# Performance work log

Measured on AMD Instinct MI355X. Metric: run time of the kernel, lower is better.

## Reference

```python
import jax, jax.numpy as jnp
import numpy as np

S, B, I, H, O = 1024, 64, 512, 2048, 512


def setup_inputs() -> dict:
    key = jax.random.key(0)
    k1, k2, k3, k4, k5 = jax.random.split(key, 5)
    X = jax.random.normal(k1, (S, B, I), dtype=jnp.float32)
    W_ih = jax.random.normal(k2, (H, I), dtype=jnp.float32) * (1.0 / np.sqrt(I))
    hh = jax.random.uniform(k3, (H,), dtype=jnp.float32)  # clamped-to-[-1,1] diagonal recurrence
    W_ho = jax.random.normal(k4, (O, H), dtype=jnp.float32) * (1.0 / np.sqrt(H))
    b_ho = jax.random.normal(k5, (O,), dtype=jnp.float32) * 0.01
    return {"X": X, "W_ih": W_ih, "hh": hh, "W_ho": W_ho, "b_ho": b_ho}


def reference(X, W_ih, hh, W_ho, b_ho):
    # Batch the input->hidden projection over the whole sequence in one GEMM:
    # u[s,b,h] = X[s,b,i] @ W_ih[h,i]^T
    u = jnp.einsum('sbi,hi->sbh', X, W_ih)
    h0 = jnp.zeros((X.shape[1], W_ih.shape[0]), dtype=X.dtype)

    def step(h, u_t):
        h_new = jnp.abs(u_t + hh * h)
        return h_new, None

    h_final, _ = jax.lax.scan(step, h0, u)
    Y = h_final @ W_ho.T + b_ho  # [B, O]
    return Y
```

## Files before the change

### kernel.cpp

```cpp
#include <hip/hip_runtime.h>
#include <hip/hip_bf16.h>
#include <stdint.h>

#define S_LEN 1024
#define B_SZ  64
#define I_SZ  512
#define H_SZ  2048
#define O_SZ  512
#define BH    (B_SZ * H_SZ)

typedef __bf16  bf16x8 __attribute__((ext_vector_type(8)));
typedef float   f32x4  __attribute__((ext_vector_type(4)));

static __device__ __forceinline__ ushort f2bf(float f) {
  union { float f; unsigned u; } v; v.f = f;
  unsigned r = v.u + 0x7FFFu + ((v.u >> 16) & 1u);
  return (ushort)(r >> 16);
}
static __device__ __forceinline__ float bf2f(ushort u) {
  return __builtin_bit_cast(float, (unsigned)u << 16);
}

#define GLOAD_LDS16(gp, lp) \
  __builtin_amdgcn_global_load_lds( \
      (__attribute__((address_space(1))) void*)(gp), \
      (__attribute__((address_space(3))) void*)(lp), 16, 0, 0)

__global__ __launch_bounds__(256) void convert_f32_bf16_kernel(
    const float4* __restrict__ in, ushort4* __restrict__ out, int n4) {
  int i = blockIdx.x * 256 + threadIdx.x;
  if (i >= n4) return;
  float4 v = in[i];
  ushort4 o; o.x = f2bf(v.x); o.y = f2bf(v.y); o.z = f2bf(v.z); o.w = f2bf(v.w);
  out[i] = o;
}

__global__ __launch_bounds__(256, 4) void fused_gemm_scan_kernel(
    const ushort* __restrict__ Xbf,
    const ushort* __restrict__ Wbf,
    const float* __restrict__ hh,
    float* __restrict__ hstate) {
  __shared__ __align__(16) ushort smem[16896];
  ushort* As = smem;
  ushort* Bs = smem + 8192;
  ushort* Cs = smem;

  const int tid  = threadIdx.x;
  const int wave = tid >> 6;
  const int lane = tid & 63;

  const int bid = blockIdx.x;
  const int x = bid & 7;
  const int g = bid >> 3;
  const int b  = (x << 3) | (g & 7);
  const int ht = g >> 3;

  const int wm = (wave >> 1) * 64;
  const int wn = (wave & 1) * 64;
  const int ml = lane & 15;
  const int q  = lane >> 4;

  const int r0     = wave * 32;
  const int srow   = lane >> 3;
  const int schunk = ((lane & 7) - srow) & 7;
  const ushort* gA0 = Xbf + ((size_t)(r0 + srow) * B_SZ + b) * I_SZ + schunk * 8;
  const ushort* gB  = Wbf + (size_t)(ht * 128 + r0 + srow) * I_SZ + schunk * 8;
  ushort* lA = As + r0 * 64;
  ushort* lB = Bs + r0 * 64;

  int swz[2];
  swz[0] = ((q + ml) & 7) * 8;
  swz[1] = ((4 + q + ml) & 7) * 8;
  int arow[4], brow[4];
  #pragma unroll
  for (int i = 0; i < 4; ++i) {
    arow[i] = (wm + i * 16 + ml) * 64;
    brow[i] = (wn + i * 16 + ml) * 64;
  }

  float c = 0.0f, hst = 0.0f;
  if (tid < 128) c = hh[ht * 128 + tid];

  for (int st = 0; st < 8; ++st) {
    f32x4 acc[4][4] = {};
    const ushort* gA = gA0 + (size_t)st * 128 * B_SZ * I_SZ;

    for (int kt = 0; kt < I_SZ / 64; ++kt) {
      __syncthreads();
      #pragma unroll
      for (int jj = 0; jj < 4; ++jj) {
        GLOAD_LDS16(gA + (size_t)(jj * 8) * B_SZ * I_SZ + kt * 64, lA + jj * 512);
        GLOAD_LDS16(gB + (size_t)(jj * 8) * I_SZ + kt * 64, lB + jj * 512);
      }
      __syncthreads();
      #pragma unroll
      for (int ks = 0; ks < 2; ++ks) {
        bf16x8 af[4], bfr[4];
        #pragma unroll
        for (int i = 0; i < 4; ++i) {
          af[i]  = *(const bf16x8*)&As[arow[i] + swz[ks]];
          bfr[i] = *(const bf16x8*)&Bs[brow[i] + swz[ks]];
        }
        #pragma unroll
        for (int mi = 0; mi < 4; ++mi)
          #pragma unroll
          for (int ni = 0; ni < 4; ++ni)
            acc[mi][ni] = __builtin_amdgcn_mfma_f32_16x16x32_bf16(
                af[mi], bfr[ni], acc[mi][ni], 0, 0, 0);
      }
    }

    __syncthreads();
    const int rl0 = wm + q * 4;
    #pragma unroll
    for (int mi = 0; mi < 4; ++mi)
      #pragma unroll
      for (int ni = 0; ni < 4; ++ni)
        #pragma unroll
        for (int r = 0; r < 4; ++r)
          Cs[(rl0 + mi * 16 + r) * 132 + wn + ni * 16 + ml] = f2bf(acc[mi][ni][r]);
    __syncthreads();

    if (tid < 128) {
      #pragma unroll
      for (int s8 = 0; s8 < 128; s8 += 8) {
        float uv[8];
        #pragma unroll
        for (int t = 0; t < 8; ++t) uv[t] = bf2f(Cs[(s8 + t) * 132 + tid]);
        #pragma unroll
        for (int t = 0; t < 8; ++t) hst = fabsf(uv[t] + c * hst);
      }
    }
  }

  if (tid < 128) hstate[(size_t)b * H_SZ + ht * 128 + tid] = hst;
}

__global__ __launch_bounds__(256) void init_y_kernel(
    const float* __restrict__ bho, float* __restrict__ Y) {
  int idx = blockIdx.x * 256 + threadIdx.x;
  Y[idx] = bho[idx & (O_SZ - 1)];
}

__global__ __launch_bounds__(256) void final_tiled_kernel(
    const float* __restrict__ hstate, const float* __restrict__ Who,
    float* __restrict__ Y) {
  __shared__ float Ws[64 * 68];
  __shared__ float Hs[64 * 68];
  const int tid = threadIdx.x;
  const int og = blockIdx.x, kc = blockIdx.y;
  const int to = tid & 15, tb = tid >> 4;
  float acc[4][4] = {};
  #pragma unroll
  for (int ks = 0; ks < 2; ++ks) {
    const int k0 = kc * 128 + ks * 64;
    const int r = tid >> 2, cg = (tid & 3) * 16;
    #pragma unroll
    for (int i2 = 0; i2 < 4; ++i2) {
      *(float4*)&Ws[r * 68 + cg + i2 * 4] =
          *(const float4*)&Who[(size_t)(og * 64 + r) * H_SZ + k0 + cg + i2 * 4];
      *(float4*)&Hs[r * 68 + cg + i2 * 4] =
          *(const float4*)&hstate[(size_t)r * H_SZ + k0 + cg + i2 * 4];
    }
    __syncthreads();
    #pragma unroll 4
    for (int k = 0; k < 64; ++k) {
      float wv[4], hv[4];
      #pragma unroll
      for (int jj2 = 0; jj2 < 4; ++jj2) wv[jj2] = Ws[(to * 4 + jj2) * 68 + k];
      #pragma unroll
      for (int ii = 0; ii < 4; ++ii) hv[ii] = Hs[(tb * 4 + ii) * 68 + k];
      #pragma unroll
      for (int ii = 0; ii < 4; ++ii)
        #pragma unroll
        for (int jj2 = 0; jj2 < 4; ++jj2)
          acc[ii][jj2] += hv[ii] * wv[jj2];
    }
    __syncthreads();
  }
  #pragma unroll
  for (int ii = 0; ii < 4; ++ii)
    #pragma unroll
    for (int jj2 = 0; jj2 < 4; ++jj2)
      atomicAdd(&Y[(size_t)(tb * 4 + ii) * O_SZ + og * 64 + to * 4 + jj2],
                acc[ii][jj2]);
}

extern "C" void kernel_launch(void* const* d_in, const int* in_sizes, int n_in,
                              void* d_out, int out_size, void* d_ws, size_t ws_size,
                              hipStream_t stream) {
  (void)in_sizes; (void)n_in; (void)out_size; (void)ws_size;
  const float* X   = (const float*)d_in[0];
  const float* Wih = (const float*)d_in[1];
  const float* hh  = (const float*)d_in[2];
  const float* Who = (const float*)d_in[3];
  const float* bho = (const float*)d_in[4];
  float* Y = (float*)d_out;

  const size_t XBF = (size_t)S_LEN * B_SZ * I_SZ * 2;
  const size_t WBF = (size_t)H_SZ * I_SZ * 2;

  char* w = (char*)d_ws;
  ushort* Xbf    = (ushort*)w;
  ushort* Wbf    = (ushort*)(w + XBF);
  float*  hstate = (float*) (w + XBF + WBF);

  {
    int n4x = (int)((size_t)S_LEN * B_SZ * I_SZ / 4);
    convert_f32_bf16_kernel<<<n4x / 256, 256, 0, stream>>>(
        (const float4*)X, (ushort4*)Xbf, n4x);
    int n4w = (int)((size_t)H_SZ * I_SZ / 4);
    convert_f32_bf16_kernel<<<n4w / 256, 256, 0, stream>>>(
        (const float4*)Wih, (ushort4*)Wbf, n4w);
  }

  fused_gemm_scan_kernel<<<1024, 256, 0, stream>>>(Xbf, Wbf, hh, hstate);

  init_y_kernel<<<(B_SZ * O_SZ) / 256, 256, 0, stream>>>(bho, Y);
  final_tiled_kernel<<<dim3(O_SZ / 64, 16), 256, 0, stream>>>(hstate, Who, Y);
}
```

Before: 414.3 us.

## Transpose X to batch-major bf16 and vectorize the scan tile layout

The bf16 conversion of X now also transposes it to [B,S,I], so each block's A-tile loads read contiguous rows instead of rows strided by B*I. The GEMM result tile is stored transposed in LDS as vectorized ushort4 writes, so each scan thread reads its column with wide loads. The recurrence is rewritten as p = fma(c, |p|, u), with the absolute value applied once at the end, which shortens the dependent chain. The transposing conversion writes with a scattered pattern, which may cost some bandwidth in that pre-pass.

```diff
diff --git a/kernel.cpp b/kernel.cpp
--- a/kernel.cpp
+++ b/kernel.cpp
@@ -25,6 +25,17 @@
   __builtin_amdgcn_global_load_lds( \
       (__attribute__((address_space(1))) void*)(gp), \
       (__attribute__((address_space(3))) void*)(lp), 16, 0, 0)
+
+__global__ __launch_bounds__(256) void convert_transpose_x_kernel(
+    const float* __restrict__ X, ushort* __restrict__ XT) {
+  int r = blockIdx.x * 2 + (threadIdx.x >> 7);
+  int t = threadIdx.x & 127;
+  int s = r >> 6, b = r & 63;
+  float4 v = *(const float4*)&X[(size_t)r * I_SZ + t * 4];
+  ushort4 o;
+  o.x = f2bf(v.x); o.y = f2bf(v.y); o.z = f2bf(v.z); o.w = f2bf(v.w);
+  *(ushort4*)&XT[((size_t)b * S_LEN + s) * I_SZ + t * 4] = o;
+}
 
 __global__ __launch_bounds__(256) void convert_f32_bf16_kernel(
     const float4* __restrict__ in, ushort4* __restrict__ out, int n4) {
@@ -36,7 +47,7 @@
 }
 
 __global__ __launch_bounds__(256, 4) void fused_gemm_scan_kernel(
-    const ushort* __restrict__ Xbf,
+    const ushort* __restrict__ XT,
     const ushort* __restrict__ Wbf,
     const float* __restrict__ hh,
     float* __restrict__ hstate) {
@@ -63,7 +74,7 @@
   const int r0     = wave * 32;
   const int srow   = lane >> 3;
   const int schunk = ((lane & 7) - srow) & 7;
-  const ushort* gA0 = Xbf + ((size_t)(r0 + srow) * B_SZ + b) * I_SZ + schunk * 8;
+  const ushort* gA0 = XT + ((size_t)b * S_LEN + r0 + srow) * I_SZ + schunk * 8;
   const ushort* gB  = Wbf + (size_t)(ht * 128 + r0 + srow) * I_SZ + schunk * 8;
   ushort* lA = As + r0 * 64;
   ushort* lB = Bs + r0 * 64;
@@ -78,18 +89,18 @@
     brow[i] = (wn + i * 16 + ml) * 64;
   }
 
-  float c = 0.0f, hst = 0.0f;
+  float c = 0.0f, p = 0.0f;
   if (tid < 128) c = hh[ht * 128 + tid];
 
   for (int st = 0; st < 8; ++st) {
     f32x4 acc[4][4] = {};
-    const ushort* gA = gA0 + (size_t)st * 128 * B_SZ * I_SZ;
+    const ushort* gA = gA0 + (size_t)st * 128 * I_SZ;
 
     for (int kt = 0; kt < I_SZ / 64; ++kt) {
       __syncthreads();
       #pragma unroll
       for (int jj = 0; jj < 4; ++jj) {
-        GLOAD_LDS16(gA + (size_t)(jj * 8) * B_SZ * I_SZ + kt * 64, lA + jj * 512);
+        GLOAD_LDS16(gA + (size_t)(jj * 8) * I_SZ + kt * 64, lA + jj * 512);
         GLOAD_LDS16(gB + (size_t)(jj * 8) * I_SZ + kt * 64, lB + jj * 512);
       }
       __syncthreads();
@@ -111,29 +122,40 @@
     }
 
     __syncthreads();
-    const int rl0 = wm + q * 4;
+    const int sb = wm + q * 4;
     #pragma unroll
-    for (int mi = 0; mi < 4; ++mi)
-      #pragma unroll
-      for (int ni = 0; ni < 4; ++ni)
-        #pragma unroll
-        for (int r = 0; r < 4; ++r)
-          Cs[(rl0 + mi * 16 + r) * 132 + wn + ni * 16 + ml] = f2bf(acc[mi][ni][r]);
+    for (int mi = 0; mi < 4; ++mi) {
+      #pragma unroll
+      for (int ni = 0; ni < 4; ++ni) {
+        ushort4 o;
+        o.x = f2bf(acc[mi][ni][0]); o.y = f2bf(acc[mi][ni][1]);
+        o.z = f2bf(acc[mi][ni][2]); o.w = f2bf(acc[mi][ni][3]);
+        *(ushort4*)&Cs[(wn + ni * 16 + ml) * 132 + sb + mi * 16] = o;
+      }
+    }
     __syncthreads();
 
     if (tid < 128) {
-      #pragma unroll
-      for (int s8 = 0; s8 < 128; s8 += 8) {
-        float uv[8];
-        #pragma unroll
-        for (int t = 0; t < 8; ++t) uv[t] = bf2f(Cs[(s8 + t) * 132 + tid]);
-        #pragma unroll
-        for (int t = 0; t < 8; ++t) hst = fabsf(uv[t] + c * hst);
-      }
-    }
-  }
-
-  if (tid < 128) hstate[(size_t)b * H_SZ + ht * 128 + tid] = hst;
+      const ushort* col = &Cs[tid * 132];
+      #pragma unroll
+      for (int s0 = 0; s0 < 128; s0 += 16) {
+        ushort4 v0 = *(const ushort4*)&col[s0];
+        ushort4 v1 = *(const ushort4*)&col[s0 + 4];
+        ushort4 v2 = *(const ushort4*)&col[s0 + 8];
+        ushort4 v3 = *(const ushort4*)&col[s0 + 12];
+        p = fmaf(c, fabsf(p), bf2f(v0.x)); p = fmaf(c, fabsf(p), bf2f(v0.y));
+        p = fmaf(c, fabsf(p), bf2f(v0.z)); p = fmaf(c, fabsf(p), bf2f(v0.w));
+        p = fmaf(c, fabsf(p), bf2f(v1.x)); p = fmaf(c, fabsf(p), bf2f(v1.y));
+        p = fmaf(c, fabsf(p), bf2f(v1.z)); p = fmaf(c, fabsf(p), bf2f(v1.w));
+        p = fmaf(c, fabsf(p), bf2f(v2.x)); p = fmaf(c, fabsf(p), bf2f(v2.y));
+        p = fmaf(c, fabsf(p), bf2f(v2.z)); p = fmaf(c, fabsf(p), bf2f(v2.w));
+        p = fmaf(c, fabsf(p), bf2f(v3.x)); p = fmaf(c, fabsf(p), bf2f(v3.y));
+        p = fmaf(c, fabsf(p), bf2f(v3.z)); p = fmaf(c, fabsf(p), bf2f(v3.w));
+      }
+    }
+  }
+
+  if (tid < 128) hstate[(size_t)b * H_SZ + ht * 128 + tid] = fabsf(p);
 }
 
 __global__ __launch_bounds__(256) void init_y_kernel(
@@ -201,20 +223,18 @@
   const size_t WBF = (size_t)H_SZ * I_SZ * 2;
 
   char* w = (char*)d_ws;
-  ushort* Xbf    = (ushort*)w;
+  ushort* XT     = (ushort*)w;
   ushort* Wbf    = (ushort*)(w + XBF);
   float*  hstate = (float*) (w + XBF + WBF);
 
+  convert_transpose_x_kernel<<<(S_LEN * B_SZ) / 2, 256, 0, stream>>>(X, XT);
   {
-    int n4x = (int)((size_t)S_LEN * B_SZ * I_SZ / 4);
-    convert_f32_bf16_kernel<<<n4x / 256, 256, 0, stream>>>(
-        (const float4*)X, (ushort4*)Xbf, n4x);
     int n4w = (int)((size_t)H_SZ * I_SZ / 4);
     convert_f32_bf16_kernel<<<n4w / 256, 256, 0, stream>>>(
         (const float4*)Wih, (ushort4*)Wbf, n4w);
   }
 
-  fused_gemm_scan_kernel<<<1024, 256, 0, stream>>>(Xbf, Wbf, hh, hstate);
+  fused_gemm_scan_kernel<<<1024, 256, 0, stream>>>(XT, Wbf, hh, hstate);
 
   init_y_kernel<<<(B_SZ * O_SZ) / 256, 256, 0, stream>>>(bho, Y);
   final_tiled_kernel<<<dim3(O_SZ / 64, 16), 256, 0, stream>>>(hstate, Who, Y);
```

Result: slower. 441.3 us (+6.5%).
